# Kernel optimization log

Hardware: AMD Instinct MI355X
Metric: run time of the kernel (lower is better)

Reference implementation:

```python
import jax, jax.numpy as jnp
import numpy as np


def _lsap_np(cost):
    """Jonker-Volgenant / Hungarian (e-maxx formulation) for a square cost
    matrix. Returns col_of_row: row i is assigned to column col_of_row[i].
    Matches scipy.optimize.linear_sum_assignment on square matrices."""
    cost = np.asarray(cost, dtype=np.float64)
    n = cost.shape[0]
    u = np.zeros(n + 1)
    v = np.zeros(n + 1)
    p = np.zeros(n + 1, dtype=np.int64)   # p[j] = row assigned to column j (1-based; 0 = none)
    way = np.zeros(n + 1, dtype=np.int64)
    for i in range(1, n + 1):
        p[0] = i
        j0 = 0
        minv = np.full(n + 1, np.inf)
        used = np.zeros(n + 1, dtype=bool)
        while True:
            used[j0] = True
            i0 = p[j0]
            js = np.nonzero(~used[1:])[0] + 1  # unused columns (vectorized inner loop)
            cur = cost[i0 - 1, js - 1] - u[i0] - v[js]
            better = cur < minv[js]
            minv[js] = np.where(better, cur, minv[js])
            way[js] = np.where(better, j0, way[js])
            j1 = js[np.argmin(minv[js])]
            delta = minv[j1]
            u[p[used]] += delta          # rows assigned to used columns are distinct
            v[used] -= delta
            minv[~used] -= delta
            j0 = j1
            if p[j0] == 0:
                break
        # augment along the alternating path
        while j0 != 0:
            j1 = way[j0]
            p[j0] = p[j1]
            j0 = j1
    col_of_row = np.zeros(n, dtype=np.int32)
    for j in range(1, n + 1):
        if p[j] > 0:
            col_of_row[p[j] - 1] = j - 1
    return col_of_row


def _batched_lsap_host(dists):
    dists = np.asarray(dists)
    return np.stack([_lsap_np(d) for d in dists]).astype(np.int32)  # [B, N]


def _pairwise_dist(y_true, y_pred):
    # dist[b, i, j] = || y_true[b, i] - y_pred[b, j] ||_2, matching tf.norm(..., axis=-1)
    diff = y_true[:, :, None, :] - y_pred[:, None, :, :]  # [B, N, N, D]
    return jnp.sqrt(jnp.sum(diff * diff, axis=-1))        # [B, N, N]


def setup_inputs() -> dict:
    key = jax.random.key(0)
    k1, k2 = jax.random.split(key)
    B, N, D = 64, 128, 64
    y_true = jax.random.normal(k1, (B, N, D), dtype=jnp.float32)
    y_pred = jax.random.normal(k2, (B, N, D), dtype=jnp.float32)
    return {"y_true": y_true, "y_pred": y_pred}


def reference(y_true, y_pred):
    dist = _pairwise_dist(y_true, y_pred)                      # [B, N, N]
    B, N = dist.shape[0], dist.shape[1]
    col_ind = jax.pure_callback(
        _batched_lsap_host,
        jax.ShapeDtypeStruct((B, N), jnp.int32),
        jax.lax.stop_gradient(dist),
    )                                                          # [B, N]
    matched = jnp.take_along_axis(dist, col_ind[:, :, None].astype(jnp.int32), axis=2)[..., 0]
    batch_losses = jnp.sum(matched, axis=1)                    # [B]
    return jnp.mean(batch_losses)
```

## Files before the change

kernel.cpp:

```cpp
#include <hip/hip_runtime.h>
#include <math.h>
#include <stdint.h>

#define BATCH 64
#define N 128
#define DIM 64
#define ARR_CAP 640

typedef unsigned uint32x2_t __attribute__((ext_vector_type(2)));

__device__ __forceinline__ unsigned monokey(float x) {
    unsigned b = __float_as_uint(x);
    return b ^ (unsigned)(((int)b >> 31) | (int)0x80000000u);
}
__device__ __forceinline__ float monoval(unsigned k) {
    unsigned b = (k & 0x80000000u) ? (k & 0x7FFFFFFFu) : ~k;
    return __uint_as_float(b);
}

__device__ __forceinline__ unsigned umin_(unsigned a, unsigned b) { return a < b ? a : b; }
__device__ __forceinline__ unsigned umax_(unsigned a, unsigned b) { return a > b ? a : b; }
__device__ __forceinline__ int rl_i(int v, int l) { return __builtin_amdgcn_readlane(v, l); }
__device__ __forceinline__ float rl_f(float v, int l) {
    return __int_as_float(__builtin_amdgcn_readlane(__float_as_int(v), l));
}

#define DPP_ROR(x, n) __builtin_amdgcn_update_dpp((int)(x), (int)(x), 0x120 + (n), 0xF, 0xF, false)

__device__ __forceinline__ unsigned partner16(unsigned x) {
#if __has_builtin(__builtin_amdgcn_permlane16_swap)
    uint32x2_t r = __builtin_amdgcn_permlane16_swap(x, x, false, false);
    return umin_(r[0], r[1]);
#else
    return umin_(x, (unsigned)__shfl_xor((int)x, 16));
#endif
}
__device__ __forceinline__ unsigned partner32(unsigned x) {
#if __has_builtin(__builtin_amdgcn_permlane32_swap)
    uint32x2_t r = __builtin_amdgcn_permlane32_swap(x, x, false, false);
    return umin_(r[0], r[1]);
#else
    return umin_(x, (unsigned)__shfl_xor((int)x, 32));
#endif
}

__device__ __forceinline__ unsigned wave_kmin(unsigned k) {
    unsigned a = (unsigned)DPP_ROR(k, 1);
    unsigned b = (unsigned)DPP_ROR(k, 2);
    k = umin_(k, umin_(a, b));
    a = (unsigned)DPP_ROR(k, 3);
    b = (unsigned)DPP_ROR(k, 6);
    k = umin_(k, umin_(a, b));
    a = (unsigned)DPP_ROR(k, 9);
    k = umin_(k, a);
    k = partner16(k);
    k = partner32(k);
    return k;
}

__device__ __forceinline__ void wave_kmin2(unsigned& ks, unsigned& kb, int lane) {
    unsigned ps, pb;
#define KM2_COMBINE { unsigned ns = umin_(ks, ps); kb = umin_(umin_(kb, pb), umax_(ks, ps)); ks = ns; }
#define KM2_SWAP16 { \
    uint32x2_t rs = __builtin_amdgcn_permlane16_swap(ks, ks, false, false); \
    uint32x2_t rb = __builtin_amdgcn_permlane16_swap(kb, kb, false, false); \
    ps = (lane & 16) ? rs[0] : rs[1]; pb = (lane & 16) ? rb[0] : rb[1]; }
#define KM2_SWAP32 { \
    uint32x2_t rs = __builtin_amdgcn_permlane32_swap(ks, ks, false, false); \
    uint32x2_t rb = __builtin_amdgcn_permlane32_swap(kb, kb, false, false); \
    ps = (lane & 32) ? rs[0] : rs[1]; pb = (lane & 32) ? rb[0] : rb[1]; }
    ps = (unsigned)DPP_ROR(ks, 1); pb = (unsigned)DPP_ROR(kb, 1); KM2_COMBINE;
    ps = (unsigned)DPP_ROR(ks, 2); pb = (unsigned)DPP_ROR(kb, 2); KM2_COMBINE;
    ps = (unsigned)DPP_ROR(ks, 4); pb = (unsigned)DPP_ROR(kb, 4); KM2_COMBINE;
    ps = (unsigned)DPP_ROR(ks, 8); pb = (unsigned)DPP_ROR(kb, 8); KM2_COMBINE;
#if __has_builtin(__builtin_amdgcn_permlane16_swap)
    KM2_SWAP16; KM2_COMBINE;
#else
    ps = (unsigned)__shfl_xor((int)ks, 16); pb = (unsigned)__shfl_xor((int)kb, 16); KM2_COMBINE;
#endif
#if __has_builtin(__builtin_amdgcn_permlane32_swap)
    KM2_SWAP32; KM2_COMBINE;
#else
    ps = (unsigned)__shfl_xor((int)ks, 32); pb = (unsigned)__shfl_xor((int)kb, 32); KM2_COMBINE;
#endif
#undef KM2_COMBINE
#undef KM2_SWAP16
#undef KM2_SWAP32
}

__global__ __launch_bounds__(64, 1)
void lsap_kernel(const float* __restrict__ y_true, const float* __restrict__ y_pred,
                 float* __restrict__ batch_sums, float* __restrict__ out, int use_atomic) {
    __shared__ float dist[N * N];
    __shared__ float ytl[N * DIM];
    __shared__ int unlist[N + ARR_CAP + 8];

    const int b = blockIdx.x;
    const int lane = threadIdx.x;
    const int ca = lane, cb = lane + 64;
    const int ja = lane + 1, jb = lane + 65;

    {
        const float4* yt4 = (const float4*)(y_true + (size_t)b * N * DIM);
        float4* ytl4 = (float4*)ytl;
        for (int k = lane; k < N * DIM / 4; k += 64) ytl4[k] = yt4[k];
    }

    float ypa[DIM], ypb[DIM];
    {
        const float4* pa4 = (const float4*)(y_pred + (size_t)b * N * DIM + (size_t)ca * DIM);
        const float4* pb4 = (const float4*)(y_pred + (size_t)b * N * DIM + (size_t)cb * DIM);
        #pragma unroll
        for (int k = 0; k < DIM / 4; ++k) {
            float4 v4 = pa4[k];
            ypa[4*k+0]=v4.x; ypa[4*k+1]=v4.y; ypa[4*k+2]=v4.z; ypa[4*k+3]=v4.w;
            float4 w4 = pb4[k];
            ypb[4*k+0]=w4.x; ypb[4*k+1]=w4.y; ypb[4*k+2]=w4.z; ypb[4*k+3]=w4.w;
        }
    }
    __syncthreads();

    float va = INFINITY, vb = INFINITY;
    for (int i = 0; i < N; ++i) {
        const float4* yr = (const float4*)(ytl + i * DIM);
        float a0 = 0.f, a1 = 0.f;
        #pragma unroll
        for (int k = 0; k < DIM / 4; ++k) {
            float4 t4 = yr[k];
            float d;
            d = t4.x - ypa[4*k+0]; a0 = fmaf(d, d, a0);
            d = t4.y - ypa[4*k+1]; a0 = fmaf(d, d, a0);
            d = t4.z - ypa[4*k+2]; a0 = fmaf(d, d, a0);
            d = t4.w - ypa[4*k+3]; a0 = fmaf(d, d, a0);
            d = t4.x - ypb[4*k+0]; a1 = fmaf(d, d, a1);
            d = t4.y - ypb[4*k+1]; a1 = fmaf(d, d, a1);
            d = t4.z - ypb[4*k+2]; a1 = fmaf(d, d, a1);
            d = t4.w - ypb[4*k+3]; a1 = fmaf(d, d, a1);
        }
        float d0 = sqrtf(a0), d1 = sqrtf(a1);
        dist[i * N + ca] = d0;
        dist[i * N + cb] = d1;
        va = fminf(va, d0);
        vb = fminf(vb, d1);
    }

    int   pa = 0, pb = 0;
    float upa = 0.f, upb = 0.f;
    float ura = 0.f, urb = 0.f;
    int   waya = 0, wayb = 0;

    int nun = 0;
    for (int r = 0; r < N; ++r) {
        float c0 = dist[r * N + ca] - va;
        float c1 = dist[r * N + cb] - vb;
        unsigned k0 = (monokey(c0) & ~0x7Fu) | (unsigned)lane;
        unsigned k1 = (monokey(c1) & ~0x7Fu) | 64u | (unsigned)lane;
        unsigned ks = umin_(k0, k1), kb2 = umax_(k0, k1);
        wave_kmin2(ks, kb2, lane);
        int s1 = __builtin_amdgcn_readfirstlane((int)ks);
        int s2 = __builtin_amdgcn_readfirstlane((int)kb2);
        float u1 = monoval((unsigned)s1 & ~0x7Fu);
        float u2 = monoval((unsigned)s2 & ~0x7Fu);
        int w1 = s1 & 63, cb1 = (s1 >> 6) & 1;
        int j1 = 1 + w1 + (cb1 << 6);
        int pj1 = rl_i(cb1 ? pb : pa, w1);
        if (pj1 == 0) {
            float dd = u2 - u1;
            if (ja == j1) { pa = r + 1; upa = u2; va -= dd; }
            if (jb == j1) { pb = r + 1; upb = u2; vb -= dd; }
            if ((r & 63) == lane) { if (r < 64) ura = u2; else urb = u2; }
        } else {
            unlist[nun] = r;
            ++nun;
            if ((r & 63) == lane) { if (r < 64) ura = u1; else urb = u1; }
        }
    }

    int k = 0, nf = nun, ops = 0, pending = -1;
    int unext = unlist[0];
    while (ops < ARR_CAP) {
        int i;
        if (pending >= 0) { i = pending; pending = -1; }
        else if (k < nf) { i = unext; ++k; unext = unlist[k]; }
        else break;
        ++ops;

        float c0 = dist[i * N + ca] - va;
        float c1 = dist[i * N + cb] - vb;
        unsigned k0 = (monokey(c0) & ~0x7Fu) | (unsigned)lane;
        unsigned k1 = (monokey(c1) & ~0x7Fu) | 64u | (unsigned)lane;
        unsigned ks = umin_(k0, k1), kb2 = umax_(k0, k1);
        wave_kmin2(ks, kb2, lane);
        int s1 = __builtin_amdgcn_readfirstlane((int)ks);
        int s2 = __builtin_amdgcn_readfirstlane((int)kb2);
        float u1 = monoval((unsigned)s1 & ~0x7Fu);
        float u2 = monoval((unsigned)s2 & ~0x7Fu);
        int w1 = s1 & 63, cb1 = (s1 >> 6) & 1;
        int w2 = s2 & 63, cb2 = (s2 >> 6) & 1;
        int j1 = 1 + w1 + (cb1 << 6);
        int j2 = 1 + w2 + (cb2 << 6);
        int pj1 = rl_i(cb1 ? pb : pa, w1);
        int pj2 = rl_i(cb2 ? pb : pa, w2);

        int jt, it0;
        if (u1 < u2) {
            float dd = u2 - u1;
            if (ja == j1) va -= dd;
            if (jb == j1) vb -= dd;
            jt = j1; it0 = pj1;
        } else if (pj1 > 0) { jt = j2; it0 = pj2; }
        else { jt = j1; it0 = 0; }

        if (ja == jt) { pa = i + 1; upa = u2; }
        if (jb == jt) { pb = i + 1; upb = u2; }
        if ((i & 63) == lane) { if (i < 64) ura = u2; else urb = u2; }

        if (it0 > 0) {
            if (u1 < u2) pending = it0 - 1;
            else {
                unlist[nf] = it0 - 1;
                if (k == nf) unext = it0 - 1;
                ++nf;
            }
        }
    }
    if (pending >= 0) { --k; unlist[k] = pending; }

    for (int t = k; t < nf; ++t) {
        int r = unlist[t];
        float u_i = rl_f((r >= 64) ? urb : ura, r & 63);
        float mina = INFINITY, minb = INFINITY;
        int useda = 0, usedb = 0;
        waya = 0; wayb = 0;
        float uacca = 0.f, uaccb = 0.f;
        float u_acc_i = u_i;
        int j0 = 0, i0 = r + 1;
        float u0c = u_i;

        for (int it = 0; it < N + 1; ++it) {
            if (ja == j0) useda = 1;
            if (jb == j0) usedb = 1;
            const float* drow = dist + (i0 - 1) * N;
            float d0 = drow[ca], d1 = drow[cb];
            if (!useda) { float cur = d0 - u0c - va; if (cur < mina) { mina = cur; waya = j0; } }
            if (!usedb) { float cur = d1 - u0c - vb; if (cur < minb) { minb = cur; wayb = j0; } }

            float candA = useda ? INFINITY : mina;
            float candB = usedb ? INFINITY : minb;
            unsigned kA = (monokey(candA) & ~0x7Fu) | (unsigned)lane;
            unsigned kB = (monokey(candB) & ~0x7Fu) | 64u | (unsigned)lane;
            unsigned kk = wave_kmin(umin_(kA, kB));
            int s = __builtin_amdgcn_readfirstlane((int)kk);
            float delta = monoval((unsigned)s & ~0x7Fu);
            int w = s & 63, cbw = (s >> 6) & 1;
            int j1 = 1 + w + (cbw << 6);
            int i1 = rl_i(cbw ? pb : pa, w);
            float u1v = rl_f(cbw ? upb : upa, w);

            if (useda) { va -= delta; uacca += delta; } else { mina -= delta; }
            if (usedb) { vb -= delta; uaccb += delta; } else { minb -= delta; }
            u_acc_i += delta;

            j0 = j1;
            if (i1 == 0) break;
            i0 = i1; u0c = u1v;
        }

        if (useda) upa += uacca;
        if (usedb) upb += uaccb;

        int jj = j0;
        for (int hop = 0; hop < N + 1; ++hop) {
            int wj = (jj - 1) & 63;
            int sbj = (jj > 64) ? 1 : 0;
            int jp = rl_i(sbj ? wayb : waya, wj);
            int np; float nu;
            if (jp == 0) { np = r + 1; nu = u_acc_i; }
            else {
                int wp = (jp - 1) & 63;
                int sbp = (jp > 64) ? 1 : 0;
                np = rl_i(sbp ? pb : pa, wp);
                nu = rl_f(sbp ? upb : upa, wp);
            }
            if (ja == jj) { pa = np; upa = nu; }
            if (jb == jj) { pb = np; upb = nu; }
            if (jp == 0) break;
            jj = jp;
        }
    }

    float s = dist[(pa - 1) * N + ca] + dist[(pb - 1) * N + cb];
    #pragma unroll
    for (int m = 1; m < 64; m <<= 1) s += __shfl_xor(s, m);
    if (lane == 0) {
        if (use_atomic) atomicAdd(out, s * (1.0f / (float)BATCH));
        else batch_sums[b] = s;
    }
}

__global__ __launch_bounds__(64)
void reduce_kernel(const float* __restrict__ bs, float* __restrict__ out) {
    int tid = threadIdx.x;
    float v = bs[tid];
    #pragma unroll
    for (int m = 1; m < 64; m <<= 1) v += __shfl_xor(v, m);
    if (tid == 0) out[0] = v * (1.0f / (float)BATCH);
}

extern "C" void kernel_launch(void* const* d_in, const int* in_sizes, int n_in,
                              void* d_out, int out_size, void* d_ws, size_t ws_size,
                              hipStream_t stream) {
    const float* y_true = (const float*)d_in[0];
    const float* y_pred = (const float*)d_in[1];
    float* out = (float*)d_out;

    if (ws_size >= BATCH * sizeof(float)) {
        float* bs = (float*)d_ws;
        lsap_kernel<<<BATCH, 64, 0, stream>>>(y_true, y_pred, bs, out, 0);
        reduce_kernel<<<1, 64, 0, stream>>>(bs, out);
    } else {
        hipMemsetAsync(d_out, 0, sizeof(float), stream);
        lsap_kernel<<<BATCH, 64, 0, stream>>>(y_true, y_pred, nullptr, out, 1);
    }
}
```

Baseline: 594.8 us.

## Pack row owner into min keys and prefetch next cost rows in LSAP loops

Packs the assigned-row index into bits of the reduction key so the wave-min result carries the owner directly, and reads exact values with readlane instead of decoding truncated keys. Next-row distance loads are issued before the reduction finishes in all three phases (column reduction, auction-like transfer, Dijkstra augmentation) to hide LDS latency. The free-row list is rebuilt with ballot/popcount from assignment flags instead of being kept in a growing array. Packing the owner into the key cuts the mantissa bits used for comparison, so tie-breaking can differ, and the augmenting loop bound is raised.

Measured after the change: 701.7 us. +18.0%, slower.

```diff
diff --git a/kernel.cpp b/kernel.cpp
--- a/kernel.cpp
+++ b/kernel.cpp
@@ -13,36 +13,16 @@
     unsigned b = __float_as_uint(x);
     return b ^ (unsigned)(((int)b >> 31) | (int)0x80000000u);
 }
-__device__ __forceinline__ float monoval(unsigned k) {
-    unsigned b = (k & 0x80000000u) ? (k & 0x7FFFFFFFu) : ~k;
-    return __uint_as_float(b);
-}
 
 __device__ __forceinline__ unsigned umin_(unsigned a, unsigned b) { return a < b ? a : b; }
 __device__ __forceinline__ unsigned umax_(unsigned a, unsigned b) { return a > b ? a : b; }
+__device__ __forceinline__ int rfl(int v) { return __builtin_amdgcn_readfirstlane(v); }
 __device__ __forceinline__ int rl_i(int v, int l) { return __builtin_amdgcn_readlane(v, l); }
 __device__ __forceinline__ float rl_f(float v, int l) {
     return __int_as_float(__builtin_amdgcn_readlane(__float_as_int(v), l));
 }
 
 #define DPP_ROR(x, n) __builtin_amdgcn_update_dpp((int)(x), (int)(x), 0x120 + (n), 0xF, 0xF, false)
-
-__device__ __forceinline__ unsigned partner16(unsigned x) {
-#if __has_builtin(__builtin_amdgcn_permlane16_swap)
-    uint32x2_t r = __builtin_amdgcn_permlane16_swap(x, x, false, false);
-    return umin_(r[0], r[1]);
-#else
-    return umin_(x, (unsigned)__shfl_xor((int)x, 16));
-#endif
-}
-__device__ __forceinline__ unsigned partner32(unsigned x) {
-#if __has_builtin(__builtin_amdgcn_permlane32_swap)
-    uint32x2_t r = __builtin_amdgcn_permlane32_swap(x, x, false, false);
-    return umin_(r[0], r[1]);
-#else
-    return umin_(x, (unsigned)__shfl_xor((int)x, 32));
-#endif
-}
 
 __device__ __forceinline__ unsigned wave_kmin(unsigned k) {
     unsigned a = (unsigned)DPP_ROR(k, 1);
@@ -53,47 +33,65 @@
     k = umin_(k, umin_(a, b));
     a = (unsigned)DPP_ROR(k, 9);
     k = umin_(k, a);
-    k = partner16(k);
-    k = partner32(k);
+#if __has_builtin(__builtin_amdgcn_permlane16_swap)
+    {
+        uint32x2_t r = __builtin_amdgcn_permlane16_swap(k, k, false, false);
+        k = umin_(r[0], r[1]);
+    }
+#else
+    k = umin_(k, (unsigned)__shfl_xor((int)k, 16));
+#endif
+#if __has_builtin(__builtin_amdgcn_permlane32_swap)
+    {
+        uint32x2_t r = __builtin_amdgcn_permlane32_swap(k, k, false, false);
+        k = umin_(r[0], r[1]);
+    }
+#else
+    k = umin_(k, (unsigned)__shfl_xor((int)k, 32));
+#endif
     return k;
 }
 
 __device__ __forceinline__ void wave_kmin2(unsigned& ks, unsigned& kb, int lane) {
     unsigned ps, pb;
 #define KM2_COMBINE { unsigned ns = umin_(ks, ps); kb = umin_(umin_(kb, pb), umax_(ks, ps)); ks = ns; }
-#define KM2_SWAP16 { \
-    uint32x2_t rs = __builtin_amdgcn_permlane16_swap(ks, ks, false, false); \
-    uint32x2_t rb = __builtin_amdgcn_permlane16_swap(kb, kb, false, false); \
-    ps = (lane & 16) ? rs[0] : rs[1]; pb = (lane & 16) ? rb[0] : rb[1]; }
-#define KM2_SWAP32 { \
-    uint32x2_t rs = __builtin_amdgcn_permlane32_swap(ks, ks, false, false); \
-    uint32x2_t rb = __builtin_amdgcn_permlane32_swap(kb, kb, false, false); \
-    ps = (lane & 32) ? rs[0] : rs[1]; pb = (lane & 32) ? rb[0] : rb[1]; }
     ps = (unsigned)DPP_ROR(ks, 1); pb = (unsigned)DPP_ROR(kb, 1); KM2_COMBINE;
     ps = (unsigned)DPP_ROR(ks, 2); pb = (unsigned)DPP_ROR(kb, 2); KM2_COMBINE;
     ps = (unsigned)DPP_ROR(ks, 4); pb = (unsigned)DPP_ROR(kb, 4); KM2_COMBINE;
     ps = (unsigned)DPP_ROR(ks, 8); pb = (unsigned)DPP_ROR(kb, 8); KM2_COMBINE;
 #if __has_builtin(__builtin_amdgcn_permlane16_swap)
-    KM2_SWAP16; KM2_COMBINE;
+    {
+        uint32x2_t rs = __builtin_amdgcn_permlane16_swap(ks, ks, false, false);
+        uint32x2_t rb = __builtin_amdgcn_permlane16_swap(kb, kb, false, false);
+        ps = (lane & 16) ? rs[0] : rs[1]; pb = (lane & 16) ? rb[0] : rb[1];
+    }
+    KM2_COMBINE;
 #else
     ps = (unsigned)__shfl_xor((int)ks, 16); pb = (unsigned)__shfl_xor((int)kb, 16); KM2_COMBINE;
 #endif
 #if __has_builtin(__builtin_amdgcn_permlane32_swap)
-    KM2_SWAP32; KM2_COMBINE;
+    {
+        uint32x2_t rs = __builtin_amdgcn_permlane32_swap(ks, ks, false, false);
+        uint32x2_t rb = __builtin_amdgcn_permlane32_swap(kb, kb, false, false);
+        ps = (lane & 32) ? rs[0] : rs[1]; pb = (lane & 32) ? rb[0] : rb[1];
+    }
+    KM2_COMBINE;
 #else
     ps = (unsigned)__shfl_xor((int)ks, 32); pb = (unsigned)__shfl_xor((int)kb, 32); KM2_COMBINE;
 #endif
 #undef KM2_COMBINE
-#undef KM2_SWAP16
-#undef KM2_SWAP32
-}
+}
+
+#define PACK_KEY(val, p, colbit, lane) \
+    ((monokey(val) & 0xFFFF8000u) | ((unsigned)(p) << 7) | ((unsigned)(colbit) << 6) | (unsigned)(lane))
 
 __global__ __launch_bounds__(64, 1)
 void lsap_kernel(const float* __restrict__ y_true, const float* __restrict__ y_pred,
                  float* __restrict__ batch_sums, float* __restrict__ out, int use_atomic) {
     __shared__ float dist[N * N];
     __shared__ float ytl[N * DIM];
-    __shared__ int unlist[N + ARR_CAP + 8];
+    __shared__ int unlist[N + 8];
+    __shared__ int flags[N];
 
     const int b = blockIdx.x;
     const int lane = threadIdx.x;
@@ -150,20 +148,20 @@
     int   waya = 0, wayb = 0;
 
     int nun = 0;
+    float pd0 = dist[ca], pd1 = dist[cb];
     for (int r = 0; r < N; ++r) {
-        float c0 = dist[r * N + ca] - va;
-        float c1 = dist[r * N + cb] - vb;
-        unsigned k0 = (monokey(c0) & ~0x7Fu) | (unsigned)lane;
-        unsigned k1 = (monokey(c1) & ~0x7Fu) | 64u | (unsigned)lane;
+        float c0 = pd0 - va, c1 = pd1 - vb;
+        if (r + 1 < N) { pd0 = dist[(r+1) * N + ca]; pd1 = dist[(r+1) * N + cb]; }
+        unsigned k0 = PACK_KEY(c0, pa, 0, lane);
+        unsigned k1 = PACK_KEY(c1, pb, 1, lane);
         unsigned ks = umin_(k0, k1), kb2 = umax_(k0, k1);
         wave_kmin2(ks, kb2, lane);
-        int s1 = __builtin_amdgcn_readfirstlane((int)ks);
-        int s2 = __builtin_amdgcn_readfirstlane((int)kb2);
-        float u1 = monoval((unsigned)s1 & ~0x7Fu);
-        float u2 = monoval((unsigned)s2 & ~0x7Fu);
-        int w1 = s1 & 63, cb1 = (s1 >> 6) & 1;
+        int s1 = rfl((int)ks);
+        int s2 = rfl((int)kb2);
+        int w1 = s1 & 63, cb1 = (s1 >> 6) & 1, pj1 = (s1 >> 7) & 0xFF;
+        float u1 = rl_f(cb1 ? c1 : c0, w1);
+        float u2 = rl_f(((s2 >> 6) & 1) ? c1 : c0, s2 & 63);
         int j1 = 1 + w1 + (cb1 << 6);
-        int pj1 = rl_i(cb1 ? pb : pa, w1);
         if (pj1 == 0) {
             float dd = u2 - u1;
             if (ja == j1) { pa = r + 1; upa = u2; va -= dd; }
@@ -176,94 +174,113 @@
         }
     }
 
-    int k = 0, nf = nun, ops = 0, pending = -1;
-    int unext = unlist[0];
-    while (ops < ARR_CAP) {
-        int i;
-        if (pending >= 0) { i = pending; pending = -1; }
-        else if (k < nf) { i = unext; ++k; unext = unlist[k]; }
-        else break;
-        ++ops;
-
-        float c0 = dist[i * N + ca] - va;
-        float c1 = dist[i * N + cb] - vb;
-        unsigned k0 = (monokey(c0) & ~0x7Fu) | (unsigned)lane;
-        unsigned k1 = (monokey(c1) & ~0x7Fu) | 64u | (unsigned)lane;
-        unsigned ks = umin_(k0, k1), kb2 = umax_(k0, k1);
-        wave_kmin2(ks, kb2, lane);
-        int s1 = __builtin_amdgcn_readfirstlane((int)ks);
-        int s2 = __builtin_amdgcn_readfirstlane((int)kb2);
-        float u1 = monoval((unsigned)s1 & ~0x7Fu);
-        float u2 = monoval((unsigned)s2 & ~0x7Fu);
-        int w1 = s1 & 63, cb1 = (s1 >> 6) & 1;
-        int w2 = s2 & 63, cb2 = (s2 >> 6) & 1;
-        int j1 = 1 + w1 + (cb1 << 6);
-        int j2 = 1 + w2 + (cb2 << 6);
-        int pj1 = rl_i(cb1 ? pb : pa, w1);
-        int pj2 = rl_i(cb2 ? pb : pa, w2);
-
-        int jt, it0;
-        if (u1 < u2) {
-            float dd = u2 - u1;
-            if (ja == j1) va -= dd;
-            if (jb == j1) vb -= dd;
-            jt = j1; it0 = pj1;
-        } else if (pj1 > 0) { jt = j2; it0 = pj2; }
-        else { jt = j1; it0 = 0; }
-
-        if (ja == jt) { pa = i + 1; upa = u2; }
-        if (jb == jt) { pb = i + 1; upb = u2; }
-        if ((i & 63) == lane) { if (i < 64) ura = u2; else urb = u2; }
-
-        if (it0 > 0) {
-            if (u1 < u2) pending = it0 - 1;
+    {
+        int k = 0;
+        int icur = -1; float d0 = 0.f, d1 = 0.f;
+        int qi = -1; float qd0 = 0.f, qd1 = 0.f;
+        if (nun > 0) {
+            icur = rfl(unlist[0]); k = 1;
+            d0 = dist[icur * N + ca]; d1 = dist[icur * N + cb];
+            if (k < nun) { qi = rfl(unlist[k]); qd0 = dist[qi * N + ca]; qd1 = dist[qi * N + cb]; }
+        }
+        int ops = 0;
+        while (icur >= 0 && ops < ARR_CAP) {
+            ++ops;
+            float c0 = d0 - va, c1 = d1 - vb;
+            unsigned k0 = PACK_KEY(c0, pa, 0, lane);
+            unsigned k1 = PACK_KEY(c1, pb, 1, lane);
+            unsigned ks = umin_(k0, k1), kb2 = umax_(k0, k1);
+            wave_kmin2(ks, kb2, lane);
+            int s1 = rfl((int)ks);
+            int s2 = rfl((int)kb2);
+            int pj1 = (s1 >> 7) & 0xFF, pj2 = (s2 >> 7) & 0xFF;
+            bool transfer = ((unsigned)s1 >> 15) < ((unsigned)s2 >> 15);
+            int it0 = transfer ? pj1 : (pj1 ? pj2 : 0);
+
+            float nd0, nd1;
+            if (it0) { nd0 = dist[(it0 - 1) * N + ca]; nd1 = dist[(it0 - 1) * N + cb]; }
+            else     { nd0 = qd0; nd1 = qd1; }
+
+            int w1 = s1 & 63, cb1 = (s1 >> 6) & 1;
+            int w2 = s2 & 63, cb2 = (s2 >> 6) & 1;
+            float u1 = rl_f(cb1 ? c1 : c0, w1);
+            float u2 = rl_f(cb2 ? c1 : c0, w2);
+            int j1 = 1 + w1 + (cb1 << 6);
+            int j2 = 1 + w2 + (cb2 << 6);
+            int jt = transfer ? j1 : (pj1 ? j2 : j1);
+            if (transfer) {
+                float dd = u2 - u1;
+                if (ja == j1) va -= dd;
+                if (jb == j1) vb -= dd;
+            }
+            if (ja == jt) { pa = icur + 1; upa = u2; }
+            if (jb == jt) { pb = icur + 1; upb = u2; }
+            if ((icur & 63) == lane) { if (icur < 64) ura = u2; else urb = u2; }
+
+            if (it0) { icur = it0 - 1; d0 = nd0; d1 = nd1; }
             else {
-                unlist[nf] = it0 - 1;
-                if (k == nf) unext = it0 - 1;
-                ++nf;
+                icur = qi; d0 = nd0; d1 = nd1;
+                if (icur >= 0) {
+                    ++k;
+                    if (k < nun) { qi = rfl(unlist[k]); qd0 = dist[qi * N + ca]; qd1 = dist[qi * N + cb]; }
+                    else qi = -1;
+                }
             }
         }
     }
-    if (pending >= 0) { --k; unlist[k] = pending; }
-
-    for (int t = k; t < nf; ++t) {
-        int r = unlist[t];
+
+    flags[lane] = 0; flags[lane + 64] = 0;
+    if (pa) flags[pa - 1] = 1;
+    if (pb) flags[pb - 1] = 1;
+    int f0 = flags[lane] ^ 1;
+    int f1 = flags[lane + 64] ^ 1;
+    unsigned long long b0 = __ballot(f0), b1 = __ballot(f1);
+    int nfree0 = __popcll(b0);
+    int nfree = nfree0 + __popcll(b1);
+    unsigned long long lt = (1ull << lane) - 1ull;
+    if (f0) unlist[__popcll(b0 & lt)] = lane;
+    if (f1) unlist[nfree0 + __popcll(b1 & lt)] = lane + 64;
+
+    for (int t = 0; t < nfree; ++t) {
+        int r = rfl(unlist[t]);
+        float d0 = dist[r * N + ca], d1 = dist[r * N + cb];
         float u_i = rl_f((r >= 64) ? urb : ura, r & 63);
         float mina = INFINITY, minb = INFINITY;
         int useda = 0, usedb = 0;
         waya = 0; wayb = 0;
         float uacca = 0.f, uaccb = 0.f;
         float u_acc_i = u_i;
-        int j0 = 0, i0 = r + 1;
         float u0c = u_i;
-
-        for (int it = 0; it < N + 1; ++it) {
+        int j0 = 0;
+
+        for (int it = 0; it < 2 * N; ++it) {
             if (ja == j0) useda = 1;
             if (jb == j0) usedb = 1;
-            const float* drow = dist + (i0 - 1) * N;
-            float d0 = drow[ca], d1 = drow[cb];
             if (!useda) { float cur = d0 - u0c - va; if (cur < mina) { mina = cur; waya = j0; } }
             if (!usedb) { float cur = d1 - u0c - vb; if (cur < minb) { minb = cur; wayb = j0; } }
 
-            float candA = useda ? INFINITY : mina;
-            float candB = usedb ? INFINITY : minb;
-            unsigned kA = (monokey(candA) & ~0x7Fu) | (unsigned)lane;
-            unsigned kB = (monokey(candB) & ~0x7Fu) | 64u | (unsigned)lane;
+            float fa = useda ? INFINITY : mina;
+            float fb = usedb ? INFINITY : minb;
+            unsigned kA = PACK_KEY(fa, pa, 0, lane);
+            unsigned kB = PACK_KEY(fb, pb, 1, lane);
             unsigned kk = wave_kmin(umin_(kA, kB));
-            int s = __builtin_amdgcn_readfirstlane((int)kk);
-            float delta = monoval((unsigned)s & ~0x7Fu);
+            int s = rfl((int)kk);
+            int i1 = (s >> 7) & 0xFF;
+
+            float nd0, nd1;
+            if (i1) { nd0 = dist[(i1 - 1) * N + ca]; nd1 = dist[(i1 - 1) * N + cb]; }
+
             int w = s & 63, cbw = (s >> 6) & 1;
-            int j1 = 1 + w + (cbw << 6);
-            int i1 = rl_i(cbw ? pb : pa, w);
+            float delta = rl_f(cbw ? fb : fa, w);
             float u1v = rl_f(cbw ? upb : upa, w);
 
             if (useda) { va -= delta; uacca += delta; } else { mina -= delta; }
             if (usedb) { vb -= delta; uaccb += delta; } else { minb -= delta; }
             u_acc_i += delta;
 
-            j0 = j1;
+            j0 = 1 + w + (cbw << 6);
             if (i1 == 0) break;
-            i0 = i1; u0c = u1v;
+            u0c = u1v; d0 = nd0; d1 = nd1;
         }
 
         if (useda) upa += uacca;
```
